# Kernel tuning notes

Hardware: AMD Instinct MI355X
Metric: run time of the kernel (lower is better)

## Reference

```python
import jax, jax.numpy as jnp
import numpy as np

N_NODES = 20000
N_EDGES = 640000


def graph_conv(x, src, dst, W, b, n_nodes):
    """DGL GraphConv with norm='both': D_in^{-1/2} A D_out^{-1/2} X W + b."""
    ones = jnp.ones(src.shape[0], dtype=x.dtype)
    deg_out = jnp.maximum(jax.ops.segment_sum(ones, src, num_segments=n_nodes), 1.0)
    deg_in = jnp.maximum(jax.ops.segment_sum(ones, dst, num_segments=n_nodes), 1.0)
    xs = x * (deg_out ** -0.5)[:, None]          # scale src features
    agg = jax.ops.segment_sum(xs[src], dst, num_segments=n_nodes)  # [N, d]
    agg = agg * (deg_in ** -0.5)[:, None]
    return agg @ W + b


def setup_inputs() -> dict:
    key = jax.random.key(0)
    ks = jax.random.split(key, 10)
    d = 256
    scale = 1.0 / np.sqrt(d)
    return {
        "x": jax.random.normal(ks[0], (N_NODES, d), dtype=jnp.float32),
        "side_src": jax.random.randint(ks[1], (N_EDGES,), 0, N_NODES),
        "side_dst": jax.random.randint(ks[2], (N_EDGES,), 0, N_NODES),
        "upd_src": jax.random.randint(ks[3], (N_EDGES,), 0, N_NODES),
        "upd_dst": jax.random.randint(ks[4], (N_EDGES,), 0, N_NODES),
        "W1_side": jax.random.normal(ks[5], (d, d), dtype=jnp.float32) * scale,
        "b1_side": jnp.zeros((d,), dtype=jnp.float32),
        "W1_upd": jax.random.normal(ks[6], (d, d), dtype=jnp.float32) * scale,
        "b1_upd": jnp.zeros((d,), dtype=jnp.float32),
        "W2_side": jax.random.normal(ks[7], (d, d), dtype=jnp.float32) * scale,
        "b2_side": jnp.zeros((d,), dtype=jnp.float32),
        "W2_upd": jax.random.normal(ks[8], (d, d), dtype=jnp.float32) * scale,
        "b2_upd": jnp.zeros((d,), dtype=jnp.float32),
    }


def reference(x, side_src, side_dst, upd_src, upd_dst,
              W1_side, b1_side, W1_upd, b1_upd,
              W2_side, b2_side, W2_upd, b2_upd):
    n = x.shape[0]
    # layer 1: HeteroGraphConv with aggregate='sum' over relations, then relu
    h = (graph_conv(x, side_src, side_dst, W1_side, b1_side, n)
         + graph_conv(x, upd_src, upd_dst, W1_upd, b1_upd, n))
    h = jax.nn.relu(h)
    # layer 2
    out = (graph_conv(h, side_src, side_dst, W2_side, b2_side, n)
           + graph_conv(h, upd_src, upd_dst, W2_upd, b2_upd, n))
    return out
```

## Files before the change

### kernel.cpp

```cpp
#include <hip/hip_runtime.h>

typedef __attribute__((ext_vector_type(8))) short short8;
typedef __attribute__((ext_vector_type(4))) float f32x4;

#define SCHUNK 2048
#define MAXN   20480
#define NSLICE 8
#define NPB    40

__device__ inline unsigned short f2bf(float v) {
    unsigned u = __float_as_uint(v);
    u += 0x7FFFu + ((u >> 16) & 1u);
    return (unsigned short)(u >> 16);
}
__device__ inline float bf2f(unsigned short h) {
    return __uint_as_float((unsigned)h << 16);
}

__global__ void bias_sum_kernel(const float* __restrict__ b1s, const float* __restrict__ b1u,
                                const float* __restrict__ b2s, const float* __restrict__ b2u,
                                float* __restrict__ bsum1, float* __restrict__ bsum2) {
    int i = threadIdx.x;
    bsum1[i] = b1s[i] + b1u[i];
    bsum2[i] = b2s[i] + b2u[i];
}

__global__ void wprep_kernel(const float* __restrict__ W1s, const float* __restrict__ W1u,
                             const float* __restrict__ W2s, const float* __restrict__ W2u,
                             unsigned short* __restrict__ Bpk1, unsigned short* __restrict__ Bpk2) {
    int k = blockIdx.x;
    int nn = threadIdx.x;
    int layer = blockIdx.y;
    const float* Ws = layer ? W2s : W1s;
    const float* Wu = layer ? W2u : W1u;
    float w = (k < 256) ? Ws[k * 256 + nn] : Wu[(k - 256) * 256 + nn];
    unsigned short hi = f2bf(w);
    unsigned short lo = f2bf(w - bf2f(hi));
    unsigned short* B = layer ? Bpk2 : Bpk1;
    size_t frag = ((size_t)(nn >> 4) * 16 + (k >> 5)) * 2;
    size_t addr = frag * 512 + ((nn & 15) + ((k >> 3) & 3) * 16) * 8 + (k & 7);
    B[addr] = hi;
    B[addr + 512] = lo;
}

__global__ __launch_bounds__(256) void hist_kernel(
    const int* __restrict__ sS, const int* __restrict__ dS,
    const int* __restrict__ sU, const int* __restrict__ dU,
    int Es, int Eu, int n, int nblk, unsigned int* __restrict__ histG) {
    __shared__ unsigned int h[MAXN];
    const int rel = blockIdx.y;
    const int* src = rel ? sU : sS;
    const int* dst = rel ? dU : dS;
    int E = rel ? Eu : Es;
    int b = blockIdx.x;
    int chunk = (E + nblk - 1) / nblk;
    int beg = b * chunk;
    int end = min(E, beg + chunk);
    for (int i = threadIdx.x; i < n; i += 256) h[i] = 0u;
    __syncthreads();
    for (int i = beg + threadIdx.x; i < end; i += 256) {
        atomicAdd(&h[src[i]], 1u);
        atomicAdd(&h[dst[i]], 0x10000u);
    }
    __syncthreads();
    unsigned int* out = histG + ((size_t)rel * nblk + b) * n;
    for (int i = threadIdx.x; i < n; i += 256) out[i] = h[i];
}

__global__ void totals_kernel(const unsigned int* __restrict__ histG, int n, int nblk,
                              float* __restrict__ sOutS, float* __restrict__ sInS,
                              float* __restrict__ sOutU, float* __restrict__ sInU,
                              int* __restrict__ degInS, int* __restrict__ degInU) {
    const int rel = blockIdx.y;
    int i = blockIdx.x * 256 + threadIdx.x;
    if (i >= n) return;
    const unsigned int* hg = histG + (size_t)rel * nblk * n;
    unsigned int lo = 0, hi = 0;
    for (int b = 0; b < nblk; ++b) {
        unsigned int v = hg[(size_t)b * n + i];
        lo += v & 0xFFFFu;
        hi += v >> 16;
    }
    float so = rsqrtf((float)(lo > 1u ? lo : 1u));
    float si = rsqrtf((float)(hi > 1u ? hi : 1u));
    if (rel) { sOutU[i] = so; sInU[i] = si; degInU[i] = (int)hi; }
    else     { sOutS[i] = so; sInS[i] = si; degInS[i] = (int)hi; }
}

__global__ __launch_bounds__(256) void scan_part_kernel(const int* __restrict__ degA,
                                                        const int* __restrict__ degB,
                                                        int n, int NB, int* __restrict__ bsum) {
    const int rel = blockIdx.y;
    const int* deg = rel ? degB : degA;
    int t = threadIdx.x;
    int base = blockIdx.x * SCHUNK + t * 8;
    int s = 0;
    if (base + 8 <= n) {
        int4 a = *(const int4*)(deg + base);
        int4 b = *(const int4*)(deg + base + 4);
        s = a.x + a.y + a.z + a.w + b.x + b.y + b.z + b.w;
    } else {
        for (int i = 0; i < 8; ++i)
            if (base + i < n) s += deg[base + i];
    }
    __shared__ int sm[256];
    sm[t] = s;
    __syncthreads();
    for (int off = 128; off > 0; off >>= 1) {
        if (t < off) sm[t] += sm[t + off];
        __syncthreads();
    }
    if (t == 0) bsum[rel * NB + blockIdx.x] = sm[0];
}

__global__ void scan_mid_kernel(int* __restrict__ bsum, int NB,
                                int* __restrict__ rpA, int* __restrict__ rpB, int n) {
    int t = threadIdx.x;
    if (t >= 2) return;
    int* bs = bsum + t * NB;
    int run = 0;
    for (int i = 0; i < NB; ++i) {
        int v = bs[i];
        bs[i] = run;
        run += v;
    }
    int* rp = t ? rpB : rpA;
    rp[n] = run;
}

__global__ __launch_bounds__(256) void scan_final_kernel(const int* __restrict__ degA,
                                                         const int* __restrict__ degB,
                                                         const int* __restrict__ bsum,
                                                         int n, int NB,
                                                         int* __restrict__ rpA,
                                                         int* __restrict__ rpB) {
    const int rel = blockIdx.y;
    const int* deg = rel ? degB : degA;
    int* rp = rel ? rpB : rpA;
    int t = threadIdx.x;
    int base = blockIdx.x * SCHUNK + t * 8;
    int v[8];
    if (base + 8 <= n) {
        int4 a = *(const int4*)(deg + base);
        int4 b = *(const int4*)(deg + base + 4);
        v[0] = a.x; v[1] = a.y; v[2] = a.z; v[3] = a.w;
        v[4] = b.x; v[5] = b.y; v[6] = b.z; v[7] = b.w;
    } else {
        for (int i = 0; i < 8; ++i) v[i] = (base + i < n) ? deg[base + i] : 0;
    }
    int s = 0;
    #pragma unroll
    for (int i = 0; i < 8; ++i) s += v[i];
    __shared__ int sm[256];
    sm[t] = s;
    __syncthreads();
    #pragma unroll
    for (int off = 1; off < 256; off <<= 1) {
        int y = (t >= off) ? sm[t - off] : 0;
        __syncthreads();
        sm[t] += y;
        __syncthreads();
    }
    int run = bsum[rel * NB + blockIdx.x] + sm[t] - s;
    #pragma unroll
    for (int i = 0; i < 8; ++i) {
        if (base + i < n) rp[base + i] = run;
        run += v[i];
    }
}

__global__ void offsets_kernel(const unsigned int* __restrict__ histG,
                               const int* __restrict__ rpS, const int* __restrict__ rpU,
                               int n, int nblk, int* __restrict__ offsG) {
    const int rel = blockIdx.y;
    int i = blockIdx.x * 256 + threadIdx.x;
    if (i >= n) return;
    const unsigned int* hg = histG + (size_t)rel * nblk * n;
    int* og = offsG + (size_t)rel * nblk * n;
    int run = (rel ? rpU : rpS)[i];
    for (int b = 0; b < nblk; ++b) {
        og[(size_t)b * n + i] = run;
        run += (int)(hg[(size_t)b * n + i] >> 16);
    }
}

__global__ __launch_bounds__(256) void csr_scatter_kernel(
    const int* __restrict__ sS, const int* __restrict__ dS,
    const int* __restrict__ sU, const int* __restrict__ dU,
    int Es, int Eu, int n, int nblk, const int* __restrict__ offsG,
    const float* __restrict__ sOutS, const float* __restrict__ sOutU,
    int2* __restrict__ csrPS, int2* __restrict__ csrPU) {
    __shared__ int off[MAXN];
    const int rel = blockIdx.y;
    const int* src = rel ? sU : sS;
    const int* dst = rel ? dU : dS;
    const float* so = rel ? sOutU : sOutS;
    int2* csrP = rel ? csrPU : csrPS;
    int E = rel ? Eu : Es;
    int b = blockIdx.x;
    int chunk = (E + nblk - 1) / nblk;
    int beg = b * chunk;
    int end = min(E, beg + chunk);
    const int* og = offsG + ((size_t)rel * nblk + b) * n;
    for (int i = threadIdx.x; i < n; i += 256) off[i] = og[i];
    __syncthreads();
    for (int i = beg + threadIdx.x; i < end; i += 256) {
        int s = src[i];
        int pos = atomicAdd(&off[dst[i]], 1);
        csrP[pos] = make_int2(s, __float_as_int(so[s]));
    }
}

__global__ __launch_bounds__(256) void pull_slice_kernel(
    const float4* __restrict__ xin,
    const int2* __restrict__ csrPS, const int2* __restrict__ csrPU,
    const int* __restrict__ rpS, const int* __restrict__ rpU,
    const float* __restrict__ sinS, const float* __restrict__ sinU,
    unsigned short* __restrict__ aggPk, int n) {
    int bid = blockIdx.x;
    int slice = bid & (NSLICE - 1);
    int rest = bid >> 3;
    int rel = rest & 1;
    int chunk = rest >> 1;
    const int2* csrP = rel ? csrPU : csrPS;
    const int* rp = rel ? rpU : rpS;
    const float* sinv = rel ? sinU : sinS;

    int wave = threadIdx.x >> 6;
    int lane = threadIdx.x & 63;
    int sub = lane >> 3;
    int sl = lane & 7;
    int fbase = slice * 8 + sl;
    int kstepg = rel * 8 + slice;

    int start = chunk * NPB;
    int lim = min(n, start + NPB);
    for (int node = start + wave; node < lim; node += 4) {
        int beg = rp[node], end = rp[node + 1];
        float ax = 0.f, ay = 0.f, az = 0.f, aw = 0.f;
        for (int eb = beg; eb < end; eb += 64) {
            int cnt = end - eb;
            if (cnt > 64) cnt = 64;
            int myu = 0;
            float myw = 0.f;
            if (lane < cnt) {
                int2 p = csrP[eb + lane];
                myu = p.x;
                myw = __int_as_float(p.y);
            }
            int jmax = (cnt + 7) >> 3;
            int j = 0;
            for (; j + 4 <= jmax; j += 4) {
                int i0 = j * 8 + sub;
                int u0 = __shfl(myu, i0);
                int u1 = __shfl(myu, i0 + 8);
                int u2 = __shfl(myu, i0 + 16);
                int u3 = __shfl(myu, i0 + 24);
                float w0 = __shfl(myw, i0);
                float w1 = __shfl(myw, i0 + 8);
                float w2 = __shfl(myw, i0 + 16);
                float w3 = __shfl(myw, i0 + 24);
                float4 a0 = xin[(size_t)u0 * 64 + fbase];
                float4 a1 = xin[(size_t)u1 * 64 + fbase];
                float4 a2 = xin[(size_t)u2 * 64 + fbase];
                float4 a3 = xin[(size_t)u3 * 64 + fbase];
                ax += w0 * a0.x + w1 * a1.x + w2 * a2.x + w3 * a3.x;
                ay += w0 * a0.y + w1 * a1.y + w2 * a2.y + w3 * a3.y;
                az += w0 * a0.z + w1 * a1.z + w2 * a2.z + w3 * a3.z;
                aw += w0 * a0.w + w1 * a1.w + w2 * a2.w + w3 * a3.w;
            }
            for (; j < jmax; ++j) {
                int idx = j * 8 + sub;
                int u = __shfl(myu, idx);
                float w = __shfl(myw, idx);
                float4 a = xin[(size_t)u * 64 + fbase];
                ax += w * a.x; ay += w * a.y; az += w * a.z; aw += w * a.w;
            }
        }
        ax += __shfl_xor(ax, 8);  ax += __shfl_xor(ax, 16); ax += __shfl_xor(ax, 32);
        ay += __shfl_xor(ay, 8);  ay += __shfl_xor(ay, 16); ay += __shfl_xor(ay, 32);
        az += __shfl_xor(az, 8);  az += __shfl_xor(az, 16); az += __shfl_xor(az, 32);
        aw += __shfl_xor(aw, 8);  aw += __shfl_xor(aw, 16); aw += __shfl_xor(aw, 32);
        if (sub == 0) {
            float si = sinv[node];
            float vx = si * ax, vy = si * ay, vz = si * az, vw = si * aw;
            ushort4 hi4 = make_ushort4(f2bf(vx), f2bf(vy), f2bf(vz), f2bf(vw));
            ushort4 lo4 = make_ushort4(f2bf(vx - bf2f(hi4.x)), f2bf(vy - bf2f(hi4.y)),
                                       f2bf(vz - bf2f(hi4.z)), f2bf(vw - bf2f(hi4.w)));
            size_t frag = ((size_t)(node >> 4) * 16 + kstepg) * 2;
            size_t addr = frag * 512 + ((node & 15) + (sl >> 1) * 16) * 8 + (sl & 1) * 4;
            *(ushort4*)&aggPk[addr] = hi4;
            *(ushort4*)&aggPk[addr + 512] = lo4;
        }
    }
}

template <int RELU>
__global__ __launch_bounds__(512) void gemm_mfma_kernel(
    const short8* __restrict__ Apk, const short8* __restrict__ Bpk,
    const float* __restrict__ bias, float* __restrict__ C, int M) {
    int lane = threadIdx.x & 63;
    int wv = threadIdx.x >> 6;
    int mt0 = blockIdx.x * 5;
    int m0 = blockIdx.x * 80;
    if (m0 >= M) return;
    int nt0 = wv * 2;
    int col0 = wv * 32;
    int frow = lane & 15;

    f32x4 acc[5][2];
    #pragma unroll
    for (int fr = 0; fr < 5; ++fr)
        #pragma unroll
        for (int fc = 0; fc < 2; ++fc)
            acc[fr][fc] = (f32x4){0.f, 0.f, 0.f, 0.f};

    #pragma unroll
    for (int ks = 0; ks < 16; ++ks) {
        short8 ah[5], al[5], bh[2], bl[2];
        #pragma unroll
        for (int fr = 0; fr < 5; ++fr) {
            size_t fa = ((size_t)(mt0 + fr) * 16 + ks) * 128 + lane;
            ah[fr] = Apk[fa];
            al[fr] = Apk[fa + 64];
        }
        #pragma unroll
        for (int fc = 0; fc < 2; ++fc) {
            size_t fb = ((size_t)(nt0 + fc) * 16 + ks) * 128 + lane;
            bh[fc] = Bpk[fb];
            bl[fc] = Bpk[fb + 64];
        }
        #pragma unroll
        for (int fr = 0; fr < 5; ++fr)
            #pragma unroll
            for (int fc = 0; fc < 2; ++fc) {
                acc[fr][fc] = __builtin_amdgcn_mfma_f32_16x16x32_bf16(ah[fr], bh[fc], acc[fr][fc], 0, 0, 0);
                acc[fr][fc] = __builtin_amdgcn_mfma_f32_16x16x32_bf16(al[fr], bh[fc], acc[fr][fc], 0, 0, 0);
                acc[fr][fc] = __builtin_amdgcn_mfma_f32_16x16x32_bf16(ah[fr], bl[fc], acc[fr][fc], 0, 0, 0);
            }
    }

    #pragma unroll
    for (int fr = 0; fr < 5; ++fr)
        #pragma unroll
        for (int fc = 0; fc < 2; ++fc) {
            int c = col0 + fc * 16 + frow;
            float bc = bias[c];
            int rb = m0 + fr * 16 + (lane >> 4) * 4;
            #pragma unroll
            for (int j = 0; j < 4; ++j) {
                int r = rb + j;
                if (r < M) {
                    float v = acc[fr][fc][j] + bc;
                    if (RELU) v = fmaxf(v, 0.f);
                    C[(size_t)r * 256 + c] = v;
                }
            }
        }
}

extern "C" void kernel_launch(void* const* d_in, const int* in_sizes, int n_in,
                              void* d_out, int out_size, void* d_ws, size_t ws_size,
                              hipStream_t stream) {
    const float* x   = (const float*)d_in[0];
    const int* sS    = (const int*)d_in[1];
    const int* dS    = (const int*)d_in[2];
    const int* sU    = (const int*)d_in[3];
    const int* dU    = (const int*)d_in[4];
    const float* W1s = (const float*)d_in[5];
    const float* b1s = (const float*)d_in[6];
    const float* W1u = (const float*)d_in[7];
    const float* b1u = (const float*)d_in[8];
    const float* W2s = (const float*)d_in[9];
    const float* b2s = (const float*)d_in[10];
    const float* W2u = (const float*)d_in[11];
    const float* b2u = (const float*)d_in[12];
    float* out = (float*)d_out;

    const int n  = in_sizes[0] / 256;
    const int Es = in_sizes[1];
    const int Eu = in_sizes[3];
    const int NB = (n + SCHUNK - 1) / SCHUNK;
    const int gemmGrid = (n + 79) / 80;
    const size_t AGG_BYTES = (size_t)gemmGrid * 5 * 16 * 2 * 512 * 2;
    const size_t BPK_BYTES = (size_t)16 * 16 * 2 * 512 * 2;

    auto plan = [&](int nb) -> size_t {
        size_t t = 0;
        auto add = [&](size_t b) { t = (t + 255) & ~(size_t)255; t += b; };
        add((size_t)2 * nb * n * 4);
        add((size_t)2 * nb * n * 4);
        add((size_t)(n + 1) * 4); add((size_t)(n + 1) * 4);
        add((size_t)n * 4); add((size_t)n * 4); add((size_t)n * 4); add((size_t)n * 4);
        add((size_t)n * 4); add((size_t)n * 4);
        add(256 * 4); add(256 * 4);
        add((size_t)2 * NB * 4);
        add((size_t)Es * 8); add((size_t)Eu * 8);
        add(2 * BPK_BYTES);
        add(AGG_BYTES);
        add((size_t)n * 256 * 4);
        return t;
    };
    const int nblk = (plan(128) <= ws_size) ? 128 : 32;

    char* ws = (char*)d_ws;
    size_t off = 0;
    auto alloc = [&](size_t bytes) -> void* {
        off = (off + 255) & ~(size_t)255;
        void* p = ws + off;
        off += bytes;
        return p;
    };

    unsigned int* histG = (unsigned int*)alloc((size_t)2 * nblk * n * 4);
    int* offsG   = (int*)alloc((size_t)2 * nblk * n * 4);
    int* rpS     = (int*)alloc((size_t)(n + 1) * 4);
    int* rpU     = (int*)alloc((size_t)(n + 1) * 4);
    float* sOutS = (float*)alloc((size_t)n * 4);
    float* sInS  = (float*)alloc((size_t)n * 4);
    float* sOutU = (float*)alloc((size_t)n * 4);
    float* sInU  = (float*)alloc((size_t)n * 4);
    int* degInS  = (int*)alloc((size_t)n * 4);
    int* degInU  = (int*)alloc((size_t)n * 4);
    float* bsum1 = (float*)alloc(256 * 4);
    float* bsum2 = (float*)alloc(256 * 4);
    int* bsumBlk = (int*)alloc((size_t)2 * NB * 4);
    int2* csrPS  = (int2*)alloc((size_t)Es * 8);
    int2* csrPU  = (int2*)alloc((size_t)Eu * 8);
    unsigned short* Bpk1 = (unsigned short*)alloc(2 * BPK_BYTES);
    unsigned short* Bpk2 = Bpk1 + BPK_BYTES / 2;
    unsigned short* aggPk = (unsigned short*)alloc(AGG_BYTES);
    float* h     = (float*)alloc((size_t)n * 256 * 4);

    bias_sum_kernel<<<1, 256, 0, stream>>>(b1s, b1u, b2s, b2u, bsum1, bsum2);
    wprep_kernel<<<dim3(512, 2), 256, 0, stream>>>(W1s, W1u, W2s, W2u, Bpk1, Bpk2);
    dim3 hg(nblk, 2);
    hist_kernel<<<hg, 256, 0, stream>>>(sS, dS, sU, dU, Es, Eu, n, nblk, histG);
    dim3 tg((n + 255) / 256, 2);
    totals_kernel<<<tg, 256, 0, stream>>>(histG, n, nblk, sOutS, sInS, sOutU, sInU,
                                          degInS, degInU);
    dim3 sg(NB, 2);
    scan_part_kernel<<<sg, 256, 0, stream>>>(degInS, degInU, n, NB, bsumBlk);
    scan_mid_kernel<<<1, 64, 0, stream>>>(bsumBlk, NB, rpS, rpU, n);
    scan_final_kernel<<<sg, 256, 0, stream>>>(degInS, degInU, bsumBlk, n, NB, rpS, rpU);
    offsets_kernel<<<tg, 256, 0, stream>>>(histG, rpS, rpU, n, nblk, offsG);
    csr_scatter_kernel<<<hg, 256, 0, stream>>>(sS, dS, sU, dU, Es, Eu, n, nblk, offsG,
                                               sOutS, sOutU, csrPS, csrPU);

    int chunks = (n + NPB - 1) / NPB;
    int pullGrid = NSLICE * 2 * chunks;
    const float4* x4 = (const float4*)x;
    const float4* h4 = (const float4*)h;
    const short8* A8 = (const short8*)aggPk;
    const short8* B81 = (const short8*)Bpk1;
    const short8* B82 = (const short8*)Bpk2;

    pull_slice_kernel<<<pullGrid, 256, 0, stream>>>(x4, csrPS, csrPU, rpS, rpU,
                                                    sInS, sInU, aggPk, n);
    gemm_mfma_kernel<1><<<gemmGrid, 512, 0, stream>>>(A8, B81, bsum1, h, n);
    pull_slice_kernel<<<pullGrid, 256, 0, stream>>>(h4, csrPS, csrPU, rpS, rpU,
                                                    sInS, sInU, aggPk, n);
    gemm_mfma_kernel<0><<<gemmGrid, 512, 0, stream>>>(A8, B82, bsum2, out, n);
}
```

Measured before the change: 484.2 us.

## Stage GEMM fragments through LDS and unroll histogram reduction loops

The MFMA GEMM now cooperatively loads the per-k-step A and B fragments into shared memory once per block, instead of each wave loading its own copies from global memory. The totals and offsets kernels unroll their strided per-block histogram loops by eight so more loads are in flight at once. The aggregation buffer size is recomputed with padding. The GEMM adds two barriers per k-step and removes the full unroll of the k loop, which could reduce overlap between loads and MFMA work.

```diff
diff --git a/kernel.cpp b/kernel.cpp
--- a/kernel.cpp
+++ b/kernel.cpp
@@ -74,10 +74,25 @@
     const int rel = blockIdx.y;
     int i = blockIdx.x * 256 + threadIdx.x;
     if (i >= n) return;
-    const unsigned int* hg = histG + (size_t)rel * nblk * n;
+    const unsigned int* hg = histG + (size_t)rel * nblk * n + i;
     unsigned int lo = 0, hi = 0;
-    for (int b = 0; b < nblk; ++b) {
-        unsigned int v = hg[(size_t)b * n + i];
+    int b = 0;
+    for (; b + 8 <= nblk; b += 8) {
+        unsigned v0 = hg[(size_t)(b + 0) * n];
+        unsigned v1 = hg[(size_t)(b + 1) * n];
+        unsigned v2 = hg[(size_t)(b + 2) * n];
+        unsigned v3 = hg[(size_t)(b + 3) * n];
+        unsigned v4 = hg[(size_t)(b + 4) * n];
+        unsigned v5 = hg[(size_t)(b + 5) * n];
+        unsigned v6 = hg[(size_t)(b + 6) * n];
+        unsigned v7 = hg[(size_t)(b + 7) * n];
+        lo += (v0 & 0xFFFFu) + (v1 & 0xFFFFu) + (v2 & 0xFFFFu) + (v3 & 0xFFFFu)
+            + (v4 & 0xFFFFu) + (v5 & 0xFFFFu) + (v6 & 0xFFFFu) + (v7 & 0xFFFFu);
+        hi += (v0 >> 16) + (v1 >> 16) + (v2 >> 16) + (v3 >> 16)
+            + (v4 >> 16) + (v5 >> 16) + (v6 >> 16) + (v7 >> 16);
+    }
+    for (; b < nblk; ++b) {
+        unsigned v = hg[(size_t)b * n];
         lo += v & 0xFFFFu;
         hi += v >> 16;
     }
@@ -175,12 +190,32 @@
     const int rel = blockIdx.y;
     int i = blockIdx.x * 256 + threadIdx.x;
     if (i >= n) return;
-    const unsigned int* hg = histG + (size_t)rel * nblk * n;
-    int* og = offsG + (size_t)rel * nblk * n;
+    const unsigned int* hg = histG + (size_t)rel * nblk * n + i;
+    int* og = offsG + (size_t)rel * nblk * n + i;
     int run = (rel ? rpU : rpS)[i];
-    for (int b = 0; b < nblk; ++b) {
-        og[(size_t)b * n + i] = run;
-        run += (int)(hg[(size_t)b * n + i] >> 16);
+    int b = 0;
+    for (; b + 8 <= nblk; b += 8) {
+        unsigned v0 = hg[(size_t)(b + 0) * n];
+        unsigned v1 = hg[(size_t)(b + 1) * n];
+        unsigned v2 = hg[(size_t)(b + 2) * n];
+        unsigned v3 = hg[(size_t)(b + 3) * n];
+        unsigned v4 = hg[(size_t)(b + 4) * n];
+        unsigned v5 = hg[(size_t)(b + 5) * n];
+        unsigned v6 = hg[(size_t)(b + 6) * n];
+        unsigned v7 = hg[(size_t)(b + 7) * n];
+        og[(size_t)(b + 0) * n] = run; run += (int)(v0 >> 16);
+        og[(size_t)(b + 1) * n] = run; run += (int)(v1 >> 16);
+        og[(size_t)(b + 2) * n] = run; run += (int)(v2 >> 16);
+        og[(size_t)(b + 3) * n] = run; run += (int)(v3 >> 16);
+        og[(size_t)(b + 4) * n] = run; run += (int)(v4 >> 16);
+        og[(size_t)(b + 5) * n] = run; run += (int)(v5 >> 16);
+        og[(size_t)(b + 6) * n] = run; run += (int)(v6 >> 16);
+        og[(size_t)(b + 7) * n] = run; run += (int)(v7 >> 16);
+    }
+    for (; b < nblk; ++b) {
+        unsigned v = hg[(size_t)b * n];
+        og[(size_t)b * n] = run;
+        run += (int)(v >> 16);
     }
 }
 
@@ -299,8 +334,10 @@
 __global__ __launch_bounds__(512) void gemm_mfma_kernel(
     const short8* __restrict__ Apk, const short8* __restrict__ Bpk,
     const float* __restrict__ bias, float* __restrict__ C, int M) {
-    int lane = threadIdx.x & 63;
-    int wv = threadIdx.x >> 6;
+    __shared__ short8 lds[42][64];
+    int tid = threadIdx.x;
+    int lane = tid & 63;
+    int wv = tid >> 6;
     int mt0 = blockIdx.x * 5;
     int m0 = blockIdx.x * 80;
     if (m0 >= M) return;
@@ -315,29 +352,41 @@
         for (int fc = 0; fc < 2; ++fc)
             acc[fr][fc] = (f32x4){0.f, 0.f, 0.f, 0.f};
 
-    #pragma unroll
     for (int ks = 0; ks < 16; ++ks) {
-        short8 ah[5], al[5], bh[2], bl[2];
+        __syncthreads();
+        #pragma unroll
+        for (int r = 0; r < 6; ++r) {
+            int s = r * 512 + tid;
+            if (s < 2688) {
+                int f = s >> 6, l = s & 63;
+                if (f < 10) {
+                    int fr = f >> 1, pl = f & 1;
+                    lds[f][l] = Apk[((size_t)(mt0 + fr) * 16 + ks) * 128 + pl * 64 + l];
+                } else {
+                    int q = f - 10;
+                    int nt = q >> 1, pl = q & 1;
+                    lds[f][l] = Bpk[((size_t)nt * 16 + ks) * 128 + pl * 64 + l];
+                }
+            }
+        }
+        __syncthreads();
+        short8 bh[2], bl[2];
+        #pragma unroll
+        for (int fc = 0; fc < 2; ++fc) {
+            bh[fc] = lds[10 + (nt0 + fc) * 2 + 0][lane];
+            bl[fc] = lds[10 + (nt0 + fc) * 2 + 1][lane];
+        }
         #pragma unroll
         for (int fr = 0; fr < 5; ++fr) {
-            size_t fa = ((size_t)(mt0 + fr) * 16 + ks) * 128 + lane;
-            ah[fr] = Apk[fa];
-            al[fr] = Apk[fa + 64];
-        }
-        #pragma unroll
-        for (int fc = 0; fc < 2; ++fc) {
-            size_t fb = ((size_t)(nt0 + fc) * 16 + ks) * 128 + lane;
-            bh[fc] = Bpk[fb];
-            bl[fc] = Bpk[fb + 64];
-        }
-        #pragma unroll
-        for (int fr = 0; fr < 5; ++fr)
+            short8 ah = lds[fr * 2 + 0][lane];
+            short8 al = lds[fr * 2 + 1][lane];
             #pragma unroll
             for (int fc = 0; fc < 2; ++fc) {
-                acc[fr][fc] = __builtin_amdgcn_mfma_f32_16x16x32_bf16(ah[fr], bh[fc], acc[fr][fc], 0, 0, 0);
-                acc[fr][fc] = __builtin_amdgcn_mfma_f32_16x16x32_bf16(al[fr], bh[fc], acc[fr][fc], 0, 0, 0);
-                acc[fr][fc] = __builtin_amdgcn_mfma_f32_16x16x32_bf16(ah[fr], bl[fc], acc[fr][fc], 0, 0, 0);
+                acc[fr][fc] = __builtin_amdgcn_mfma_f32_16x16x32_bf16(ah, bh[fc], acc[fr][fc], 0, 0, 0);
+                acc[fr][fc] = __builtin_amdgcn_mfma_f32_16x16x32_bf16(al, bh[fc], acc[fr][fc], 0, 0, 0);
+                acc[fr][fc] = __builtin_amdgcn_mfma_f32_16x16x32_bf16(ah, bl[fc], acc[fr][fc], 0, 0, 0);
             }
+        }
     }
 
     #pragma unroll
@@ -382,7 +431,7 @@
     const int Eu = in_sizes[3];
     const int NB = (n + SCHUNK - 1) / SCHUNK;
     const int gemmGrid = (n + 79) / 80;
-    const size_t AGG_BYTES = (size_t)gemmGrid * 5 * 16 * 2 * 512 * 2;
+    const size_t AGG_BYTES = (size_t)((n + 15) / 16 + 16) * 16 * 2 * 512 * 2;
     const size_t BPK_BYTES = (size_t)16 * 16 * 2 * 512 * 2;
 
     auto plan = [&](int nb) -> size_t {
```

Result: faster. 456.6 us (-5.7%).
